# Optimization experiments

Measured on AMD Instinct MI355X. Metric: run time of the kernel, lower is better.

The kernel has to match this reference:

```python
import jax, jax.numpy as jnp
import numpy as np

N, DIM, EMB = 8192, 128, 16
WIDTHS = [64, 32, 16]


def setup_inputs() -> dict:
    key = jax.random.key(0)
    ks = jax.random.split(key, 16)
    x = jax.random.normal(ks[0], (N, DIM), dtype=jnp.float32)
    dims = [DIM] + WIDTHS + [EMB]  # 128 -> 64 -> 32 -> 16 -> 16
    params = {}
    for i in range(4):
        fan_in, fan_out = dims[i], dims[i + 1]
        params[f"W{i+1}"] = jax.random.normal(ks[1 + 2 * i], (fan_in, fan_out), dtype=jnp.float32) * (1.0 / np.sqrt(fan_in))
        params[f"b{i+1}"] = jax.random.normal(ks[2 + 2 * i], (fan_out,), dtype=jnp.float32) * 0.01
    return {"x": x, **params}


def _encode(x, W1, b1, W2, b2, W3, b3, W4, b4):
    h = jax.nn.relu(x @ W1 + b1)
    h = jax.nn.relu(h @ W2 + b2)
    h = jax.nn.relu(h @ W3 + b3)
    return h @ W4 + b4  # [N, EMB]


def _tstudent_probs(z):
    # squared euclidean distances via the norm trick (avoids [N,N,EMB] tensor)
    sq = jnp.sum(z * z, axis=1)  # [N]
    dist = jnp.maximum(sq[:, None] + sq[None, :] - 2.0 * (z @ z.T), 0.0)  # [N,N]
    numerator = 1.0 / (1.0 + dist)
    return numerator / jnp.sum(numerator, axis=1, keepdims=True)


def reference(x, W1, b1, W2, b2, W3, b3, W4, b4):
    z = _encode(x, W1, b1, W2, b2, W3, b3, W4, b4)
    return _tstudent_probs(z)
```

## Files before the change

kernel.cpp:

```cpp
#include <hip/hip_runtime.h>

#define N 8192
#define DIM 128
#define NCHUNK 32

__global__ __launch_bounds__(64) void encoder_kernel(
    const float* __restrict__ x,
    const float* __restrict__ W1, const float* __restrict__ b1,
    const float* __restrict__ W2, const float* __restrict__ b2,
    const float* __restrict__ W3, const float* __restrict__ b3,
    const float* __restrict__ W4, const float* __restrict__ b4,
    float* __restrict__ z, float* __restrict__ sqout)
{
    __shared__ float sW2[64 * 32];
    __shared__ float sW3[32 * 16];
    __shared__ float sW4[16 * 16];
    __shared__ float sb1[64];
    __shared__ float sb2[32];
    __shared__ float sb3[16];
    __shared__ float sb4[16];
    __shared__ float sW1[128 * 64];
    __shared__ float sh1[64 * 65];

    int t = threadIdx.x;
    float* sh2 = sW1;
    float* sh3 = sW1 + 2112;

    for (int idx = t; idx < 128 * 64; idx += 64) sW1[idx] = W1[idx];
    for (int idx = t; idx < 64 * 32; idx += 64) sW2[idx] = W2[idx];
    for (int idx = t; idx < 32 * 16; idx += 64) sW3[idx] = W3[idx];
    for (int idx = t; idx < 16 * 16; idx += 64) sW4[idx] = W4[idx];
    sb1[t] = b1[t];
    if (t < 32) sb2[t] = b2[t];
    if (t < 16) { sb3[t] = b3[t]; sb4[t] = b4[t]; }
    __syncthreads();

    int row = blockIdx.x * 64 + t;
    const float4* xr = (const float4*)(x + (size_t)row * DIM);

    float h1[64];
    #pragma unroll
    for (int k = 0; k < 64; ++k) h1[k] = sb1[k];
    for (int j4 = 0; j4 < 32; ++j4) {
        float4 xv = xr[j4];
        const float* w0 = &sW1[(j4 * 4 + 0) * 64];
        const float* w1 = &sW1[(j4 * 4 + 1) * 64];
        const float* w2 = &sW1[(j4 * 4 + 2) * 64];
        const float* w3 = &sW1[(j4 * 4 + 3) * 64];
        #pragma unroll
        for (int k = 0; k < 64; ++k) h1[k] = fmaf(xv.x, w0[k], h1[k]);
        #pragma unroll
        for (int k = 0; k < 64; ++k) h1[k] = fmaf(xv.y, w1[k], h1[k]);
        #pragma unroll
        for (int k = 0; k < 64; ++k) h1[k] = fmaf(xv.z, w2[k], h1[k]);
        #pragma unroll
        for (int k = 0; k < 64; ++k) h1[k] = fmaf(xv.w, w3[k], h1[k]);
    }
    #pragma unroll
    for (int k = 0; k < 64; ++k) sh1[t * 65 + k] = fmaxf(h1[k], 0.0f);

    float h2[32];
    #pragma unroll
    for (int k = 0; k < 32; ++k) h2[k] = sb2[k];
    for (int j = 0; j < 64; ++j) {
        float a = sh1[t * 65 + j];
        #pragma unroll
        for (int k = 0; k < 32; ++k) h2[k] = fmaf(a, sW2[j * 32 + k], h2[k]);
    }
    #pragma unroll
    for (int k = 0; k < 32; ++k) sh2[t * 33 + k] = fmaxf(h2[k], 0.0f);

    float h3[16];
    #pragma unroll
    for (int k = 0; k < 16; ++k) h3[k] = sb3[k];
    for (int j = 0; j < 32; ++j) {
        float a = sh2[t * 33 + j];
        #pragma unroll
        for (int k = 0; k < 16; ++k) h3[k] = fmaf(a, sW3[j * 16 + k], h3[k]);
    }
    #pragma unroll
    for (int k = 0; k < 16; ++k) sh3[t * 17 + k] = fmaxf(h3[k], 0.0f);

    float zo[16];
    #pragma unroll
    for (int k = 0; k < 16; ++k) zo[k] = sb4[k];
    for (int j = 0; j < 16; ++j) {
        float a = sh3[t * 17 + j];
        #pragma unroll
        for (int k = 0; k < 16; ++k) zo[k] = fmaf(a, sW4[j * 16 + k], zo[k]);
    }

    float s = 0.0f;
    #pragma unroll
    for (int k = 0; k < 16; ++k) s = fmaf(zo[k], zo[k], s);
    sqout[row] = s;
    float4* zr = (float4*)(z + (size_t)row * 16);
    zr[0] = make_float4(zo[0], zo[1], zo[2], zo[3]);
    zr[1] = make_float4(zo[4], zo[5], zo[6], zo[7]);
    zr[2] = make_float4(zo[8], zo[9], zo[10], zo[11]);
    zr[3] = make_float4(zo[12], zo[13], zo[14], zo[15]);
}

__global__ __launch_bounds__(256) void pass1_kernel(
    const float* __restrict__ z, const float* __restrict__ sq,
    float* __restrict__ partial)
{
    __shared__ float s_zj[256 * 16];
    __shared__ float s_sqj[256];

    int t = threadIdx.x;
    int i0 = blockIdx.x * 256 + t;
    int i1 = i0 + 4096;
    int jb = blockIdx.y * 256;

    {
        const float4* src = (const float4*)(z + (size_t)(jb + t) * 16);
        float4* dst = (float4*)(s_zj + t * 16);
        dst[0] = src[0]; dst[1] = src[1]; dst[2] = src[2]; dst[3] = src[3];
        s_sqj[t] = sq[jb + t];
    }

    float zi0[16], zi1[16];
    {
        const float4* p0 = (const float4*)(z + (size_t)i0 * 16);
        const float4* p1 = (const float4*)(z + (size_t)i1 * 16);
        #pragma unroll
        for (int q = 0; q < 4; ++q) {
            float4 v0 = p0[q]; float4 v1 = p1[q];
            zi0[4*q] = v0.x; zi0[4*q+1] = v0.y; zi0[4*q+2] = v0.z; zi0[4*q+3] = v0.w;
            zi1[4*q] = v1.x; zi1[4*q+1] = v1.y; zi1[4*q+2] = v1.z; zi1[4*q+3] = v1.w;
        }
    }
    float sqi0 = sq[i0], sqi1 = sq[i1];
    __syncthreads();

    float acc0 = 0.0f, acc1 = 0.0f;
    #pragma unroll 4
    for (int jj = 0; jj < 256; ++jj) {
        const float* zj = s_zj + jj * 16;
        float d0 = 0.0f, d1 = 0.0f;
        #pragma unroll
        for (int k = 0; k < 16; ++k) {
            float w = zj[k];
            d0 = fmaf(zi0[k], w, d0);
            d1 = fmaf(zi1[k], w, d1);
        }
        float sj = s_sqj[jj];
        float dist0 = fmaxf(fmaf(-2.0f, d0, sqi0 + sj), 0.0f);
        float dist1 = fmaxf(fmaf(-2.0f, d1, sqi1 + sj), 0.0f);
        acc0 += __builtin_amdgcn_rcpf(1.0f + dist0);
        acc1 += __builtin_amdgcn_rcpf(1.0f + dist1);
    }
    partial[blockIdx.y * N + i0] = acc0;
    partial[blockIdx.y * N + i1] = acc1;
}

__global__ __launch_bounds__(256) void pass2_kernel(
    const float* __restrict__ z, const float* __restrict__ sq,
    const float* __restrict__ partial, float* __restrict__ out)
{
    __shared__ float s_zi[16 * 16];
    __shared__ float s_sqi[16];
    __shared__ float s_inv[16];
    __shared__ float s_red[16 * NCHUNK];

    int t = threadIdx.x;
    int ibase = blockIdx.x * 16;

    s_zi[t] = z[(size_t)ibase * 16 + t];
    if (t < 16) s_sqi[t] = sq[ibase + t];
    for (int q = t; q < 16 * NCHUNK; q += 256) {
        int ii = q >> 5;
        int c  = q & (NCHUNK - 1);
        s_red[ii * NCHUNK + c] = partial[(size_t)c * N + ibase + ii];
    }
    __syncthreads();
    if (t < 16) {
        float s = 0.0f;
        #pragma unroll
        for (int c = 0; c < NCHUNK; ++c) s += s_red[t * NCHUNK + c];
        s_inv[t] = 1.0f / s;
    }
    __syncthreads();

    for (int jb = 0; jb < N; jb += 256) {
        int j = jb + t;
        float zj[16];
        {
            const float4* zp = (const float4*)(z + (size_t)j * 16);
            #pragma unroll
            for (int q = 0; q < 4; ++q) {
                float4 v = zp[q];
                zj[4*q] = v.x; zj[4*q+1] = v.y; zj[4*q+2] = v.z; zj[4*q+3] = v.w;
            }
        }
        float sqj = sq[j];
        #pragma unroll
        for (int ii = 0; ii < 16; ++ii) {
            const float* zi = s_zi + ii * 16;
            float d = 0.0f;
            #pragma unroll
            for (int k = 0; k < 16; ++k) d = fmaf(zi[k], zj[k], d);
            float dist = fmaxf(fmaf(-2.0f, d, s_sqi[ii] + sqj), 0.0f);
            float num = __builtin_amdgcn_rcpf(1.0f + dist);
            __builtin_nontemporal_store(num * s_inv[ii],
                                        &out[(size_t)(ibase + ii) * N + j]);
        }
    }
}

extern "C" void kernel_launch(void* const* d_in, const int* in_sizes, int n_in,
                              void* d_out, int out_size, void* d_ws, size_t ws_size,
                              hipStream_t stream) {
    const float* x  = (const float*)d_in[0];
    const float* W1 = (const float*)d_in[1];
    const float* b1 = (const float*)d_in[2];
    const float* W2 = (const float*)d_in[3];
    const float* b2 = (const float*)d_in[4];
    const float* W3 = (const float*)d_in[5];
    const float* b3 = (const float*)d_in[6];
    const float* W4 = (const float*)d_in[7];
    const float* b4 = (const float*)d_in[8];
    float* out = (float*)d_out;

    float* ws = (float*)d_ws;
    float* z       = ws;
    float* sq      = ws + N * 16;
    float* partial = ws + N * 16 + N;

    encoder_kernel<<<128, 64, 0, stream>>>(x, W1, b1, W2, b2, W3, b3, W4, b4, z, sq);
    pass1_kernel<<<dim3(16, NCHUNK), 256, 0, stream>>>(z, sq, partial);
    pass2_kernel<<<N / 16, 256, 0, stream>>>(z, sq, partial, out);
}
```

Baseline: 395.6 us.

## Use transposed z layout and float4 stores in output pass

The encoder now also writes a column-major copy of z, so the output pass can load four consecutive j values per dimension as vectors and emit 16-byte nontemporal stores. Each block now covers 4 rows instead of 16, which gives 2048 blocks, and the per-row partial sums are reduced with a wave shuffle instead of a shared-memory loop. The aim is wider, better-coalesced writes of the 256 MB output and fewer per-element loads. In exchange it adds extra workspace and scattered strided writes of zT in the encoder, and reloads zT more often because each block handles fewer rows.

```diff
diff --git a/kernel.cpp b/kernel.cpp
--- a/kernel.cpp
+++ b/kernel.cpp
@@ -3,6 +3,8 @@
 #define N 8192
 #define DIM 128
 #define NCHUNK 32
+
+typedef float f32x4 __attribute__((ext_vector_type(4)));
 
 __global__ __launch_bounds__(64) void encoder_kernel(
     const float* __restrict__ x,
@@ -10,7 +12,7 @@
     const float* __restrict__ W2, const float* __restrict__ b2,
     const float* __restrict__ W3, const float* __restrict__ b3,
     const float* __restrict__ W4, const float* __restrict__ b4,
-    float* __restrict__ z, float* __restrict__ sqout)
+    float* __restrict__ z, float* __restrict__ zT, float* __restrict__ sqout)
 {
     __shared__ float sW2[64 * 32];
     __shared__ float sW3[32 * 16];
@@ -99,6 +101,8 @@
     zr[1] = make_float4(zo[4], zo[5], zo[6], zo[7]);
     zr[2] = make_float4(zo[8], zo[9], zo[10], zo[11]);
     zr[3] = make_float4(zo[12], zo[13], zo[14], zo[15]);
+    #pragma unroll
+    for (int k = 0; k < 16; ++k) zT[(size_t)k * N + row] = zo[k];
 }
 
 __global__ __launch_bounds__(256) void pass1_kernel(
@@ -156,55 +160,62 @@
 }
 
 __global__ __launch_bounds__(256) void pass2_kernel(
-    const float* __restrict__ z, const float* __restrict__ sq,
+    const float* __restrict__ z, const float* __restrict__ zT,
+    const float* __restrict__ sq,
     const float* __restrict__ partial, float* __restrict__ out)
 {
-    __shared__ float s_zi[16 * 16];
-    __shared__ float s_sqi[16];
-    __shared__ float s_inv[16];
-    __shared__ float s_red[16 * NCHUNK];
+    __shared__ float s_inv[4];
 
     int t = threadIdx.x;
-    int ibase = blockIdx.x * 16;
-
-    s_zi[t] = z[(size_t)ibase * 16 + t];
-    if (t < 16) s_sqi[t] = sq[ibase + t];
-    for (int q = t; q < 16 * NCHUNK; q += 256) {
-        int ii = q >> 5;
-        int c  = q & (NCHUNK - 1);
-        s_red[ii * NCHUNK + c] = partial[(size_t)c * N + ibase + ii];
+    int ibase = blockIdx.x * 4;
+    int w = t >> 6, lane = t & 63;
+
+    {
+        float v = (lane < NCHUNK) ? partial[(size_t)lane * N + ibase + w] : 0.0f;
+        #pragma unroll
+        for (int off = 32; off > 0; off >>= 1) v += __shfl_xor(v, off, 64);
+        if (lane == 0) s_inv[w] = 1.0f / v;
+    }
+
+    float zi[4][16];
+    float sqi[4];
+    #pragma unroll
+    for (int rr = 0; rr < 4; ++rr) {
+        const float4* p = (const float4*)(z + (size_t)(ibase + rr) * 16);
+        #pragma unroll
+        for (int q = 0; q < 4; ++q) {
+            float4 v = p[q];
+            zi[rr][4*q]   = v.x; zi[rr][4*q+1] = v.y;
+            zi[rr][4*q+2] = v.z; zi[rr][4*q+3] = v.w;
+        }
+        sqi[rr] = sq[ibase + rr];
     }
     __syncthreads();
-    if (t < 16) {
-        float s = 0.0f;
-        #pragma unroll
-        for (int c = 0; c < NCHUNK; ++c) s += s_red[t * NCHUNK + c];
-        s_inv[t] = 1.0f / s;
-    }
-    __syncthreads();
-
-    for (int jb = 0; jb < N; jb += 256) {
-        int j = jb + t;
-        float zj[16];
-        {
-            const float4* zp = (const float4*)(z + (size_t)j * 16);
+    float inv[4];
+    #pragma unroll
+    for (int rr = 0; rr < 4; ++rr) inv[rr] = s_inv[rr];
+
+    for (int jb = 0; jb < N; jb += 1024) {
+        int j0 = jb + t * 4;
+        f32x4 zjT[16];
+        #pragma unroll
+        for (int k = 0; k < 16; ++k)
+            zjT[k] = *(const f32x4*)(zT + (size_t)k * N + j0);
+        f32x4 sqj = *(const f32x4*)(sq + j0);
+
+        #pragma unroll
+        for (int rr = 0; rr < 4; ++rr) {
+            f32x4 d = {0.0f, 0.0f, 0.0f, 0.0f};
             #pragma unroll
-            for (int q = 0; q < 4; ++q) {
-                float4 v = zp[q];
-                zj[4*q] = v.x; zj[4*q+1] = v.y; zj[4*q+2] = v.z; zj[4*q+3] = v.w;
-            }
-        }
-        float sqj = sq[j];
-        #pragma unroll
-        for (int ii = 0; ii < 16; ++ii) {
-            const float* zi = s_zi + ii * 16;
-            float d = 0.0f;
-            #pragma unroll
-            for (int k = 0; k < 16; ++k) d = fmaf(zi[k], zj[k], d);
-            float dist = fmaxf(fmaf(-2.0f, d, s_sqi[ii] + sqj), 0.0f);
-            float num = __builtin_amdgcn_rcpf(1.0f + dist);
-            __builtin_nontemporal_store(num * s_inv[ii],
-                                        &out[(size_t)(ibase + ii) * N + j]);
+            for (int k = 0; k < 16; ++k) d += zi[rr][k] * zjT[k];
+            f32x4 dist = sqi[rr] + sqj - 2.0f * d;
+            f32x4 num;
+            num.x = __builtin_amdgcn_rcpf(1.0f + fmaxf(dist.x, 0.0f)) * inv[rr];
+            num.y = __builtin_amdgcn_rcpf(1.0f + fmaxf(dist.y, 0.0f)) * inv[rr];
+            num.z = __builtin_amdgcn_rcpf(1.0f + fmaxf(dist.z, 0.0f)) * inv[rr];
+            num.w = __builtin_amdgcn_rcpf(1.0f + fmaxf(dist.w, 0.0f)) * inv[rr];
+            __builtin_nontemporal_store(num,
+                (f32x4*)(out + (size_t)(ibase + rr) * N + j0));
         }
     }
 }
@@ -225,10 +236,11 @@
 
     float* ws = (float*)d_ws;
     float* z       = ws;
-    float* sq      = ws + N * 16;
-    float* partial = ws + N * 16 + N;
-
-    encoder_kernel<<<128, 64, 0, stream>>>(x, W1, b1, W2, b2, W3, b3, W4, b4, z, sq);
-    pass1_kernel<<<dim3(16, NCHUNK), 256, 0, stream>>>(z, sq, partial);
-    pass2_kernel<<<N / 16, 256, 0, stream>>>(z, sq, partial, out);
-}
+    float* zT      = ws + N * 16;
+    float* sqv     = ws + N * 32;
+    float* partial = ws + N * 32 + N;
+
+    encoder_kernel<<<128, 64, 0, stream>>>(x, W1, b1, W2, b2, W3, b3, W4, b4, z, zT, sqv);
+    pass1_kernel<<<dim3(16, NCHUNK), 256, 0, stream>>>(z, sqv, partial);
+    pass2_kernel<<<N / 4, 256, 0, stream>>>(z, zT, sqv, partial, out);
+}
```

Result: faster. 376.9 us (-4.7%).
